# Kernel optimization log

Measured on AMD Instinct MI355X. Metric: run time of the kernel, lower is better.

## Reference

```python
import jax, jax.numpy as jnp
import numpy as np

BN_EPS = 1e-5


def setup_inputs() -> dict:
    key = jax.random.key(0)
    ks = jax.random.split(key, 9)
    B, C, H, W = 2, 64, 128, 128
    Ci = 32  # inter_channels
    sc = 0.05
    x = jax.random.normal(ks[0], (B, C, H, W), jnp.float32)
    g_w = jax.random.normal(ks[1], (Ci, C), jnp.float32) * sc
    g_b = jax.random.normal(ks[2], (Ci,), jnp.float32) * sc
    theta_w = jax.random.normal(ks[3], (Ci, C), jnp.float32) * sc
    theta_b = jax.random.normal(ks[4], (Ci,), jnp.float32) * sc
    phi_w = jax.random.normal(ks[5], (Ci, C), jnp.float32) * sc
    phi_b = jax.random.normal(ks[6], (Ci,), jnp.float32) * sc
    w_w = jax.random.normal(ks[7], (C, Ci), jnp.float32) * sc
    w_b = jnp.zeros((C,), jnp.float32)
    # BatchNorm affine params (random so the block is non-trivial; the torch
    # code zero-inits them, which would make the whole block an identity).
    bn_gamma = 1.0 + 0.1 * jax.random.normal(ks[8], (C,), jnp.float32)
    bn_beta = jnp.zeros((C,), jnp.float32)
    return dict(x=x, g_w=g_w, g_b=g_b, theta_w=theta_w, theta_b=theta_b,
                phi_w=phi_w, phi_b=phi_b, w_w=w_w, w_b=w_b,
                bn_gamma=bn_gamma, bn_beta=bn_beta)


def reference(x, g_w, g_b, theta_w, theta_b, phi_w, phi_b, w_w, w_b,
              bn_gamma, bn_beta):
    B, C, H, W = x.shape
    Ci = g_w.shape[0]
    H1, W1 = H // 2, W // 2

    def block(xq):  # embedded-gaussian non-local block on one quadrant group [B,C,h,w]
        b, c, h, w = xq.shape
        n = h * w
        xf = xq.reshape(b, c, n)                                  # [B,C,N]
        th = jnp.einsum('oc,bcn->bno', theta_w, xf) + theta_b     # [B,N,Ci]
        ph = jnp.einsum('oc,bcn->bon', phi_w, xf) + phi_b[:, None]  # [B,Ci,N]
        gx = jnp.einsum('oc,bcn->bno', g_w, xf) + g_b             # [B,N,Ci]
        f = jnp.einsum('bno,bom->bnm', th, ph)                    # [B,N,N] affinity
        a = jax.nn.softmax(f, axis=-1)
        y = jnp.einsum('bnm,bmo->bno', a, gx)                     # [B,N,Ci]
        wy = jnp.einsum('co,bno->bcn', w_w, y) + w_b[:, None]     # [B,C,N]
        wy = wy.reshape(b, c, h, w)
        # BatchNorm2d, training-mode batch stats (per quadrant call in torch)
        mu = wy.mean(axis=(0, 2, 3), keepdims=True)
        var = wy.var(axis=(0, 2, 3), keepdims=True)
        bn = (wy - mu) * jax.lax.rsqrt(var + BN_EPS)
        bn = bn * bn_gamma[None, :, None, None] + bn_beta[None, :, None, None]
        return bn + xq                                            # residual

    # split into 4 quadrants: [B,C,H,W] -> [4,B,C,H1,W1] (quadrant-major)
    xq = x.reshape(B, C, 2, H1, 2, W1).transpose(2, 4, 0, 1, 3, 5)
    xq = xq.reshape(4, B, C, H1, W1)
    zq = jax.vmap(block)(xq)                                      # [4,B,C,H1,W1]
    # reassemble
    z = zq.reshape(2, 2, B, C, H1, W1).transpose(2, 3, 0, 4, 1, 5)
    return z.reshape(B, C, H, W)
```

## Files before the change

### kernel.cpp

```cpp
#include <hip/hip_runtime.h>
#include <stdint.h>

typedef __bf16 bf16x8 __attribute__((ext_vector_type(8)));
typedef short  short4v __attribute__((ext_vector_type(4)));
typedef float  floatx4 __attribute__((ext_vector_type(4)));
typedef uint32_t u32x4 __attribute__((ext_vector_type(4)));

#define DI __device__ __forceinline__

DI uint16_t bf1(float a) {
    union { __bf16 h; uint16_t u; } r; r.h = (__bf16)a; return r.u;
}

__global__ __launch_bounds__(256) void proj_kernel(
    const float* __restrict__ x,
    const float* __restrict__ tw, const float* __restrict__ tb,
    const float* __restrict__ pw, const float* __restrict__ pb,
    const float* __restrict__ gw, const float* __restrict__ gb,
    uint16_t* __restrict__ th, uint16_t* __restrict__ phT,
    uint16_t* __restrict__ vP)
{
    __shared__ uint16_t ldsg[32 * 68];
    int nt = blockIdx.x & 63, blk = blockIdx.x >> 6;
    int tid = threadIdx.x, wid = tid >> 6, lane = tid & 63;
    int quad = lane >> 4, low = lane & 15;

    int b = blk & 1, q = blk >> 1, qh = q >> 1, qw = q & 1;
    int pixA = wid * 16 + low;
    const float* xg = x + (size_t)b * 1048576 +
                      (size_t)(qh * 64 + nt) * 128 + qw * 64 + pixA;

    float a0[8], a1[8];
#pragma unroll
    for (int j = 0; j < 8; ++j) {
        a0[j] = xg[(size_t)(quad * 8 + j) * 16384];
        a1[j] = xg[(size_t)(32 + quad * 8 + j) * 16384];
    }
    bf16x8 A0, A1;
#pragma unroll
    for (int j = 0; j < 8; ++j) {
        A0[j] = (__bf16)a0[j];
        A1[j] = (__bf16)a1[j];
    }

    auto dotile = [&](const float* W, const float* Bv, int o0) -> floatx4 {
        floatx4 acc;
        float bias = Bv[o0 + low];
#pragma unroll
        for (int r = 0; r < 4; ++r) acc[r] = bias;
        const float* wr = W + (o0 + low) * 64 + quad * 8;
        floatx4 w0a = *(const floatx4*)(wr);
        floatx4 w0b = *(const floatx4*)(wr + 4);
        floatx4 w1a = *(const floatx4*)(wr + 32);
        floatx4 w1b = *(const floatx4*)(wr + 36);
        bf16x8 B0, B1;
#pragma unroll
        for (int j = 0; j < 4; ++j) {
            B0[j]     = (__bf16)w0a[j];
            B0[j + 4] = (__bf16)w0b[j];
            B1[j]     = (__bf16)w1a[j];
            B1[j + 4] = (__bf16)w1b[j];
        }
        acc = __builtin_amdgcn_mfma_f32_16x16x32_bf16(A0, B0, acc, 0, 0, 0);
        acc = __builtin_amdgcn_mfma_f32_16x16x32_bf16(A1, B1, acc, 0, 0, 0);
        return acc;
    };

    size_t thbase = ((size_t)blk * 4096 + nt * 64 + wid * 16 + quad * 4) * 32;

    floatx4 t0 = dotile(tw, tb, 0), t1 = dotile(tw, tb, 16);
#pragma unroll
    for (int r = 0; r < 4; ++r) {
        th[thbase + r * 32 + low]      = bf1(t0[r] * 1.44269504088896f);
        th[thbase + r * 32 + 16 + low] = bf1(t1[r] * 1.44269504088896f);
    }
    floatx4 p0 = dotile(pw, pb, 0), p1 = dotile(pw, pb, 16);
#pragma unroll
    for (int r = 0; r < 4; ++r) {
        phT[thbase + r * 32 + low]      = bf1(p0[r]);
        phT[thbase + r * 32 + 16 + low] = bf1(p1[r]);
    }
    floatx4 g0 = dotile(gw, gb, 0), g1 = dotile(gw, gb, 16);
#pragma unroll
    for (int r = 0; r < 4; ++r) {
        ldsg[(low)      * 68 + wid * 16 + quad * 4 + r] = bf1(g0[r]);
        ldsg[(16 + low) * 68 + wid * 16 + quad * 4 + r] = bf1(g1[r]);
    }
    __syncthreads();
    {
        int o = tid >> 3, k = (tid & 7) * 8;
        const uint16_t* src = &ldsg[o * 68 + k];
        uint64_t lo = *(const uint64_t*)(src);
        uint64_t hi = *(const uint64_t*)(src + 4);
        union { uint64_t q[2]; u32x4 v; } out;
        out.q[0] = lo; out.q[1] = hi;
        *(u32x4*)(vP + (size_t)blk * 131072 + nt * 2048 + tid * 8) = out.v;
    }
}

__global__ __launch_bounds__(512, 4) void flash_kernel(
    const uint16_t* __restrict__ th, const uint16_t* __restrict__ phT,
    const uint16_t* __restrict__ vP, const float* __restrict__ w_w,
    const float* __restrict__ w_b, float* __restrict__ wy,
    float2* __restrict__ partials)
{
    __shared__ uint16_t ldsK[2][2][2][64 * 40];
    __shared__ uint16_t ldsV[2][2][2][32 * 72];
    __shared__ float sred[4][64][2];
    int blk = blockIdx.x & 7;
    int rg  = blockIdx.x >> 3;
    int tid = threadIdx.x, wid = tid >> 6, lane = tid & 63;
    int half = wid >> 2, w4 = wid & 3;
    int ltid = tid & 255;
    int quad = lane >> 4, low = lane & 15;
    int n0 = rg * 64 + w4 * 16;
    int sstag = wid & 1;

    const uint16_t* thB = th  + (size_t)blk * 131072;
    const uint16_t* kG  = phT + (size_t)blk * 131072;
    const uint16_t* vG  = vP  + (size_t)blk * 131072;

    bf16x8 qf = *(const bf16x8*)(thB + (n0 + low) * 32 + quad * 8);

    const int kWr = (ltid >> 2) * 40 + (ltid & 3) * 8;
    const int vWr = (ltid >> 3) * 72 + (ltid & 7) * 8;
    const u32x4* kSrc = (const u32x4*)kG + half * 8192 + ltid;
    const u32x4* vSrc = (const u32x4*)vG + half * 8192 + ltid;

    u32x4 kr0 = kSrc[0],  kr1 = kSrc[256];
    u32x4 vr0 = vSrc[0],  vr1 = vSrc[256];
    *(u32x4*)(&ldsK[half][0][0][kWr]) = kr0;  *(u32x4*)(&ldsK[half][0][1][kWr]) = kr1;
    *(u32x4*)(&ldsV[half][0][0][vWr]) = vr0;  *(u32x4*)(&ldsV[half][0][1][vWr]) = vr1;
    __syncthreads();

    floatx4 zero = {0.f, 0.f, 0.f, 0.f};
    floatx4 oa0 = zero, oa1 = zero, os = zero;
    union { uint32_t u[2]; short4v v; } ones;
    ones.u[0] = 0x3F803F80u; ones.u[1] = 0x3F803F80u;

    for (int t = 0; t < 16; ++t) {
        int buf = t & 1;
        if (t < 15) {
            kr0 = kSrc[(2*t + 2) * 256]; kr1 = kSrc[(2*t + 3) * 256];
            vr0 = vSrc[(2*t + 2) * 256]; vr1 = vSrc[(2*t + 3) * 256];
        }
#pragma unroll
        for (int si = 0; si < 2; ++si) {
            int s = si ^ sstag;
            const uint16_t* Kb = ldsK[half][buf][s];
            const uint16_t* Vb = ldsV[half][buf][s];
            bf16x8  kf[4]; short4v va[4], vb[4];
#pragma unroll
            for (int c = 0; c < 4; ++c) {
                kf[c] = *(const bf16x8*)(Kb + (c * 16 + low) * 40 + quad * 8);
                va[c] = *(const short4v*)(Vb + low * 72 + c * 16 + quad * 4);
                vb[c] = *(const short4v*)(Vb + (16 + low) * 72 + c * 16 + quad * 4);
            }
            floatx4 sa[4];
#pragma unroll
            for (int c = 0; c < 4; ++c)
                sa[c] = __builtin_amdgcn_mfma_f32_16x16x32_bf16(kf[c], qf, zero, 0, 0, 0);
            union { __bf16 h[4]; short4v v; } P[4];
#pragma unroll
            for (int c = 0; c < 4; ++c) {
                float p0 = __builtin_amdgcn_exp2f(sa[c][0]);
                float p1 = __builtin_amdgcn_exp2f(sa[c][1]);
                float p2 = __builtin_amdgcn_exp2f(sa[c][2]);
                float p3 = __builtin_amdgcn_exp2f(sa[c][3]);
                P[c].h[0] = (__bf16)p0; P[c].h[1] = (__bf16)p1;
                P[c].h[2] = (__bf16)p2; P[c].h[3] = (__bf16)p3;
            }
#pragma unroll
            for (int c = 0; c < 4; ++c) {
                oa0 = __builtin_amdgcn_mfma_f32_16x16x16bf16_1k(va[c], P[c].v, oa0, 0, 0, 0);
                oa1 = __builtin_amdgcn_mfma_f32_16x16x16bf16_1k(vb[c], P[c].v, oa1, 0, 0, 0);
                os  = __builtin_amdgcn_mfma_f32_16x16x16bf16_1k(ones.v, P[c].v, os, 0, 0, 0);
            }
        }
        if (t < 15) {
            *(u32x4*)(&ldsK[half][buf ^ 1][0][kWr]) = kr0;
            *(u32x4*)(&ldsK[half][buf ^ 1][1][kWr]) = kr1;
            *(u32x4*)(&ldsV[half][buf ^ 1][0][vWr]) = vr0;
            *(u32x4*)(&ldsV[half][buf ^ 1][1][vWr]) = vr1;
        }
        __syncthreads();
    }

    {
        float* exM = (float*)(&ldsK[half][0][0][0]);
        int li9 = ltid * 9;
#pragma unroll
        for (int r = 0; r < 4; ++r) {
            exM[li9 + r]     = oa0[r];
            exM[li9 + 4 + r] = oa1[r];
        }
        exM[li9 + 8] = os[0];
    }
    __syncthreads();
    const float* exO = (const float*)(&ldsK[half ^ 1][0][0][0]);
    float os0 = os[0] + exO[ltid * 9 + 8];
#pragma unroll
    for (int r = 0; r < 4; ++r) {
        oa0[r] += exO[ltid * 9 + r];
        oa1[r] += exO[ltid * 9 + 4 + r];
    }

    float rinv = 1.0f / os0;
    union { __bf16 h[4]; short4v v; } Y0, Y1;
#pragma unroll
    for (int r = 0; r < 4; ++r) {
        Y0.h[r] = (__bf16)(oa0[r] * rinv);
        Y1.h[r] = (__bf16)(oa1[r] * rinv);
    }

    float* wyB = wy + (size_t)blk * 262144;
    int n = n0 + low;
#pragma unroll
    for (int cc = 0; cc < 2; ++cc) {
        int ct = half * 2 + cc;
        floatx4 acc;
#pragma unroll
        for (int r = 0; r < 4; ++r) acc[r] = w_b[ct * 16 + quad * 4 + r];
        floatx4 w0 = *(const floatx4*)(w_w + (ct * 16 + low) * 32 + quad * 4);
        floatx4 w1 = *(const floatx4*)(w_w + (ct * 16 + low) * 32 + 16 + quad * 4);
        union { __bf16 h[4]; short4v v; } W0, W1;
#pragma unroll
        for (int r = 0; r < 4; ++r) {
            W0.h[r] = (__bf16)w0[r];
            W1.h[r] = (__bf16)w1[r];
        }
        acc = __builtin_amdgcn_mfma_f32_16x16x16bf16_1k(W0.v, Y0.v, acc, 0, 0, 0);
        acc = __builtin_amdgcn_mfma_f32_16x16x16bf16_1k(W1.v, Y1.v, acc, 0, 0, 0);
#pragma unroll
        for (int r = 0; r < 4; ++r) {
            wyB[(size_t)(ct * 16 + quad * 4 + r) * 4096 + n] = acc[r];
            float s = acc[r], ss = acc[r] * acc[r];
            s += __shfl_xor(s, 1); ss += __shfl_xor(ss, 1);
            s += __shfl_xor(s, 2); ss += __shfl_xor(ss, 2);
            s += __shfl_xor(s, 4); ss += __shfl_xor(ss, 4);
            s += __shfl_xor(s, 8); ss += __shfl_xor(ss, 8);
            if (low == 0) {
                sred[w4][ct * 16 + quad * 4 + r][0] = s;
                sred[w4][ct * 16 + quad * 4 + r][1] = ss;
            }
        }
    }
    __syncthreads();
    if (tid < 64) {
        float s  = sred[0][tid][0] + sred[1][tid][0] + sred[2][tid][0] + sred[3][tid][0];
        float ss = sred[0][tid][1] + sred[1][tid][1] + sred[2][tid][1] + sred[3][tid][1];
        partials[((size_t)blk * 64 + rg) * 64 + tid] = make_float2(s, ss);
    }
}

__global__ __launch_bounds__(256) void stats_kernel(
    const float2* __restrict__ partials, const float* __restrict__ gamma,
    const float* __restrict__ beta, float2* __restrict__ stats)
{
    int q = blockIdx.x;
    int c = threadIdx.x & 63, g = threadIdx.x >> 6;
    float S = 0.f, SS = 0.f;
    for (int w = g; w < 128; w += 4) {
        int wg = (q * 2 + (w >> 6)) * 64 + (w & 63);
        float2 p = partials[(size_t)wg * 64 + c];
        S += p.x; SS += p.y;
    }
    __shared__ float sh[2][4][64];
    sh[0][g][c] = S; sh[1][g][c] = SS;
    __syncthreads();
    if (threadIdx.x < 64) {
        int cc = threadIdx.x;
        float St  = sh[0][0][cc] + sh[0][1][cc] + sh[0][2][cc] + sh[0][3][cc];
        float SSt = sh[1][0][cc] + sh[1][1][cc] + sh[1][2][cc] + sh[1][3][cc];
        float mu  = St * (1.0f / 8192.0f);
        float var = SSt * (1.0f / 8192.0f) - mu * mu;
        float scale = gamma[cc] * rsqrtf(var + 1e-5f);
        float shift = beta[cc] - mu * scale;
        stats[q * 64 + cc] = make_float2(scale, shift);
    }
}

__global__ __launch_bounds__(256) void final_kernel(
    const float* __restrict__ wy, const float2* __restrict__ stats,
    const float* __restrict__ x, float* __restrict__ out)
{
    size_t base = ((size_t)blockIdx.x * 256 + threadIdx.x) * 4;
    int n   = (int)(base & 4095);
    int c   = (int)((base >> 12) & 63);
    int blk = (int)(base >> 18);
    int b = blk & 1, q = blk >> 1, qh = q >> 1, qw = q & 1;
    int i = n >> 6, j = n & 63;
    float2 sc = stats[q * 64 + c];
    floatx4 wv = *(const floatx4*)(wy + base);
    size_t xa = ((size_t)(b * 64 + c) * 128 + (qh * 64 + i)) * 128 + qw * 64 + j;
    floatx4 xv = *(const floatx4*)(x + xa);
    floatx4 ov;
#pragma unroll
    for (int k = 0; k < 4; ++k) ov[k] = wv[k] * sc.x + sc.y + xv[k];
    *(floatx4*)(out + xa) = ov;
}

extern "C" void kernel_launch(void* const* d_in, const int* in_sizes, int n_in,
                              void* d_out, int out_size, void* d_ws, size_t ws_size,
                              hipStream_t stream)
{
    const float* x       = (const float*)d_in[0];
    const float* g_w     = (const float*)d_in[1];
    const float* g_b     = (const float*)d_in[2];
    const float* theta_w = (const float*)d_in[3];
    const float* theta_b = (const float*)d_in[4];
    const float* phi_w   = (const float*)d_in[5];
    const float* phi_b   = (const float*)d_in[6];
    const float* w_w     = (const float*)d_in[7];
    const float* w_b     = (const float*)d_in[8];
    const float* gamma   = (const float*)d_in[9];
    const float* beta    = (const float*)d_in[10];

    char* ws = (char*)d_ws;
    uint16_t* th       = (uint16_t*)(ws);
    uint16_t* phT      = (uint16_t*)(ws + (2u << 20));
    uint16_t* vP       = (uint16_t*)(ws + (4u << 20));
    float*    wy       = (float*)(ws + (6u << 20));
    float2*   partials = (float2*)(ws + (14u << 20));
    float2*   stats    = (float2*)(ws + (14u << 20) + (1u << 18));

    proj_kernel  <<<512,  256, 0, stream>>>(x, theta_w, theta_b, phi_w, phi_b,
                                            g_w, g_b, th, phT, vP);
    flash_kernel <<<512,  512, 0, stream>>>(th, phT, vP, w_w, w_b, wy, partials);
    stats_kernel <<<4,    256, 0, stream>>>(partials, gamma, beta, stats);
    final_kernel <<<2048, 256, 0, stream>>>(wy, stats, x, (float*)d_out);
}
```

Measured before the change: 139.5 us.

## Process two query tiles per wave in flash kernel to reuse K/V fragments

Each wave now handles 32 query rows (two 16-row tiles) instead of 16, so every K and V fragment loaded from LDS feeds twice as many MFMAs. The grid is halved to 256 blocks and launch bounds are relaxed to allow more registers. The stats kernel is rewritten as one 64-thread block per channel/quadrant doing a shuffle reduction over the smaller partials array. The trade is fewer blocks and higher register pressure, which lowers occupancy on a 256-CU device, and the per-wave staggering of the LDS sub-tile order is removed.

```diff
diff --git a/kernel.cpp b/kernel.cpp
--- a/kernel.cpp
+++ b/kernel.cpp
@@ -98,7 +98,7 @@
     }
 }
 
-__global__ __launch_bounds__(512, 4) void flash_kernel(
+__global__ __launch_bounds__(512, 2) void flash_kernel(
     const uint16_t* __restrict__ th, const uint16_t* __restrict__ phT,
     const uint16_t* __restrict__ vP, const float* __restrict__ w_w,
     const float* __restrict__ w_b, float* __restrict__ wy,
@@ -113,14 +113,14 @@
     int half = wid >> 2, w4 = wid & 3;
     int ltid = tid & 255;
     int quad = lane >> 4, low = lane & 15;
-    int n0 = rg * 64 + w4 * 16;
-    int sstag = wid & 1;
+    int n0 = rg * 128 + w4 * 32;
 
     const uint16_t* thB = th  + (size_t)blk * 131072;
     const uint16_t* kG  = phT + (size_t)blk * 131072;
     const uint16_t* vG  = vP  + (size_t)blk * 131072;
 
-    bf16x8 qf = *(const bf16x8*)(thB + (n0 + low) * 32 + quad * 8);
+    bf16x8 qfA = *(const bf16x8*)(thB + (n0 + low) * 32 + quad * 8);
+    bf16x8 qfB = *(const bf16x8*)(thB + (n0 + 16 + low) * 32 + quad * 8);
 
     const int kWr = (ltid >> 2) * 40 + (ltid & 3) * 8;
     const int vWr = (ltid >> 3) * 72 + (ltid & 7) * 8;
@@ -134,7 +134,8 @@
     __syncthreads();
 
     floatx4 zero = {0.f, 0.f, 0.f, 0.f};
-    floatx4 oa0 = zero, oa1 = zero, os = zero;
+    floatx4 oaA0 = zero, oaA1 = zero, osA = zero;
+    floatx4 oaB0 = zero, oaB1 = zero, osB = zero;
     union { uint32_t u[2]; short4v v; } ones;
     ones.u[0] = 0x3F803F80u; ones.u[1] = 0x3F803F80u;
 
@@ -145,8 +146,7 @@
             vr0 = vSrc[(2*t + 2) * 256]; vr1 = vSrc[(2*t + 3) * 256];
         }
 #pragma unroll
-        for (int si = 0; si < 2; ++si) {
-            int s = si ^ sstag;
+        for (int s = 0; s < 2; ++s) {
             const uint16_t* Kb = ldsK[half][buf][s];
             const uint16_t* Vb = ldsV[half][buf][s];
             bf16x8  kf[4]; short4v va[4], vb[4];
@@ -156,25 +156,32 @@
                 va[c] = *(const short4v*)(Vb + low * 72 + c * 16 + quad * 4);
                 vb[c] = *(const short4v*)(Vb + (16 + low) * 72 + c * 16 + quad * 4);
             }
-            floatx4 sa[4];
-#pragma unroll
-            for (int c = 0; c < 4; ++c)
-                sa[c] = __builtin_amdgcn_mfma_f32_16x16x32_bf16(kf[c], qf, zero, 0, 0, 0);
-            union { __bf16 h[4]; short4v v; } P[4];
+            floatx4 saA[4], saB[4];
 #pragma unroll
             for (int c = 0; c < 4; ++c) {
-                float p0 = __builtin_amdgcn_exp2f(sa[c][0]);
-                float p1 = __builtin_amdgcn_exp2f(sa[c][1]);
-                float p2 = __builtin_amdgcn_exp2f(sa[c][2]);
-                float p3 = __builtin_amdgcn_exp2f(sa[c][3]);
-                P[c].h[0] = (__bf16)p0; P[c].h[1] = (__bf16)p1;
-                P[c].h[2] = (__bf16)p2; P[c].h[3] = (__bf16)p3;
-            }
+                saA[c] = __builtin_amdgcn_mfma_f32_16x16x32_bf16(kf[c], qfA, zero, 0, 0, 0);
+                saB[c] = __builtin_amdgcn_mfma_f32_16x16x32_bf16(kf[c], qfB, zero, 0, 0, 0);
+            }
+            union { __bf16 h[4]; short4v v; } PA[4], PB[4];
 #pragma unroll
             for (int c = 0; c < 4; ++c) {
-                oa0 = __builtin_amdgcn_mfma_f32_16x16x16bf16_1k(va[c], P[c].v, oa0, 0, 0, 0);
-                oa1 = __builtin_amdgcn_mfma_f32_16x16x16bf16_1k(vb[c], P[c].v, oa1, 0, 0, 0);
-                os  = __builtin_amdgcn_mfma_f32_16x16x16bf16_1k(ones.v, P[c].v, os, 0, 0, 0);
+                PA[c].h[0] = (__bf16)__builtin_amdgcn_exp2f(saA[c][0]);
+                PA[c].h[1] = (__bf16)__builtin_amdgcn_exp2f(saA[c][1]);
+                PA[c].h[2] = (__bf16)__builtin_amdgcn_exp2f(saA[c][2]);
+                PA[c].h[3] = (__bf16)__builtin_amdgcn_exp2f(saA[c][3]);
+                PB[c].h[0] = (__bf16)__builtin_amdgcn_exp2f(saB[c][0]);
+                PB[c].h[1] = (__bf16)__builtin_amdgcn_exp2f(saB[c][1]);
+                PB[c].h[2] = (__bf16)__builtin_amdgcn_exp2f(saB[c][2]);
+                PB[c].h[3] = (__bf16)__builtin_amdgcn_exp2f(saB[c][3]);
+            }
+#pragma unroll
+            for (int c = 0; c < 4; ++c) {
+                oaA0 = __builtin_amdgcn_mfma_f32_16x16x16bf16_1k(va[c], PA[c].v, oaA0, 0, 0, 0);
+                oaB0 = __builtin_amdgcn_mfma_f32_16x16x16bf16_1k(va[c], PB[c].v, oaB0, 0, 0, 0);
+                oaA1 = __builtin_amdgcn_mfma_f32_16x16x16bf16_1k(vb[c], PA[c].v, oaA1, 0, 0, 0);
+                oaB1 = __builtin_amdgcn_mfma_f32_16x16x16bf16_1k(vb[c], PB[c].v, oaB1, 0, 0, 0);
+                osA  = __builtin_amdgcn_mfma_f32_16x16x16bf16_1k(ones.v, PA[c].v, osA, 0, 0, 0);
+                osB  = __builtin_amdgcn_mfma_f32_16x16x16bf16_1k(ones.v, PB[c].v, osB, 0, 0, 0);
             }
         }
         if (t < 15) {
@@ -188,39 +195,50 @@
 
     {
         float* exM = (float*)(&ldsK[half][0][0][0]);
-        int li9 = ltid * 9;
+        int li = ltid * 18;
 #pragma unroll
         for (int r = 0; r < 4; ++r) {
-            exM[li9 + r]     = oa0[r];
-            exM[li9 + 4 + r] = oa1[r];
-        }
-        exM[li9 + 8] = os[0];
+            exM[li + r]      = oaA0[r];
+            exM[li + 4 + r]  = oaA1[r];
+            exM[li + 9 + r]  = oaB0[r];
+            exM[li + 13 + r] = oaB1[r];
+        }
+        exM[li + 8]  = osA[0];
+        exM[li + 17] = osB[0];
     }
     __syncthreads();
     const float* exO = (const float*)(&ldsK[half ^ 1][0][0][0]);
-    float os0 = os[0] + exO[ltid * 9 + 8];
-#pragma unroll
-    for (int r = 0; r < 4; ++r) {
-        oa0[r] += exO[ltid * 9 + r];
-        oa1[r] += exO[ltid * 9 + 4 + r];
-    }
-
-    float rinv = 1.0f / os0;
-    union { __bf16 h[4]; short4v v; } Y0, Y1;
-#pragma unroll
-    for (int r = 0; r < 4; ++r) {
-        Y0.h[r] = (__bf16)(oa0[r] * rinv);
-        Y1.h[r] = (__bf16)(oa1[r] * rinv);
+    float osA0 = osA[0] + exO[ltid * 18 + 8];
+    float osB0 = osB[0] + exO[ltid * 18 + 17];
+#pragma unroll
+    for (int r = 0; r < 4; ++r) {
+        oaA0[r] += exO[ltid * 18 + r];
+        oaA1[r] += exO[ltid * 18 + 4 + r];
+        oaB0[r] += exO[ltid * 18 + 9 + r];
+        oaB1[r] += exO[ltid * 18 + 13 + r];
+    }
+
+    float rinvA = 1.0f / osA0, rinvB = 1.0f / osB0;
+    union { __bf16 h[4]; short4v v; } YA0, YA1, YB0, YB1;
+#pragma unroll
+    for (int r = 0; r < 4; ++r) {
+        YA0.h[r] = (__bf16)(oaA0[r] * rinvA);
+        YA1.h[r] = (__bf16)(oaA1[r] * rinvA);
+        YB0.h[r] = (__bf16)(oaB0[r] * rinvB);
+        YB1.h[r] = (__bf16)(oaB1[r] * rinvB);
     }
 
     float* wyB = wy + (size_t)blk * 262144;
-    int n = n0 + low;
+    int nA = n0 + low, nB = n0 + 16 + low;
 #pragma unroll
     for (int cc = 0; cc < 2; ++cc) {
         int ct = half * 2 + cc;
-        floatx4 acc;
-#pragma unroll
-        for (int r = 0; r < 4; ++r) acc[r] = w_b[ct * 16 + quad * 4 + r];
+        floatx4 accA, accB;
+#pragma unroll
+        for (int r = 0; r < 4; ++r) {
+            accA[r] = w_b[ct * 16 + quad * 4 + r];
+            accB[r] = accA[r];
+        }
         floatx4 w0 = *(const floatx4*)(w_w + (ct * 16 + low) * 32 + quad * 4);
         floatx4 w1 = *(const floatx4*)(w_w + (ct * 16 + low) * 32 + 16 + quad * 4);
         union { __bf16 h[4]; short4v v; } W0, W1;
@@ -229,19 +247,24 @@
             W0.h[r] = (__bf16)w0[r];
             W1.h[r] = (__bf16)w1[r];
         }
-        acc = __builtin_amdgcn_mfma_f32_16x16x16bf16_1k(W0.v, Y0.v, acc, 0, 0, 0);
-        acc = __builtin_amdgcn_mfma_f32_16x16x16bf16_1k(W1.v, Y1.v, acc, 0, 0, 0);
+        accA = __builtin_amdgcn_mfma_f32_16x16x16bf16_1k(W0.v, YA0.v, accA, 0, 0, 0);
+        accA = __builtin_amdgcn_mfma_f32_16x16x16bf16_1k(W1.v, YA1.v, accA, 0, 0, 0);
+        accB = __builtin_amdgcn_mfma_f32_16x16x16bf16_1k(W0.v, YB0.v, accB, 0, 0, 0);
+        accB = __builtin_amdgcn_mfma_f32_16x16x16bf16_1k(W1.v, YB1.v, accB, 0, 0, 0);
 #pragma unroll
         for (int r = 0; r < 4; ++r) {
-            wyB[(size_t)(ct * 16 + quad * 4 + r) * 4096 + n] = acc[r];
-            float s = acc[r], ss = acc[r] * acc[r];
+            int ch = ct * 16 + quad * 4 + r;
+            wyB[(size_t)ch * 4096 + nA] = accA[r];
+            wyB[(size_t)ch * 4096 + nB] = accB[r];
+            float s = accA[r] + accB[r];
+            float ss = accA[r] * accA[r] + accB[r] * accB[r];
             s += __shfl_xor(s, 1); ss += __shfl_xor(ss, 1);
             s += __shfl_xor(s, 2); ss += __shfl_xor(ss, 2);
             s += __shfl_xor(s, 4); ss += __shfl_xor(ss, 4);
             s += __shfl_xor(s, 8); ss += __shfl_xor(ss, 8);
             if (low == 0) {
-                sred[w4][ct * 16 + quad * 4 + r][0] = s;
-                sred[w4][ct * 16 + quad * 4 + r][1] = ss;
+                sred[w4][ch][0] = s;
+                sred[w4][ch][1] = ss;
             }
         }
     }
@@ -249,34 +272,32 @@
     if (tid < 64) {
         float s  = sred[0][tid][0] + sred[1][tid][0] + sred[2][tid][0] + sred[3][tid][0];
         float ss = sred[0][tid][1] + sred[1][tid][1] + sred[2][tid][1] + sred[3][tid][1];
-        partials[((size_t)blk * 64 + rg) * 64 + tid] = make_float2(s, ss);
-    }
-}
-
-__global__ __launch_bounds__(256) void stats_kernel(
+        partials[((size_t)blk * 32 + rg) * 64 + tid] = make_float2(s, ss);
+    }
+}
+
+__global__ __launch_bounds__(64) void stats_kernel(
     const float2* __restrict__ partials, const float* __restrict__ gamma,
     const float* __restrict__ beta, float2* __restrict__ stats)
 {
-    int q = blockIdx.x;
-    int c = threadIdx.x & 63, g = threadIdx.x >> 6;
-    float S = 0.f, SS = 0.f;
-    for (int w = g; w < 128; w += 4) {
-        int wg = (q * 2 + (w >> 6)) * 64 + (w & 63);
-        float2 p = partials[(size_t)wg * 64 + c];
-        S += p.x; SS += p.y;
-    }
-    __shared__ float sh[2][4][64];
-    sh[0][g][c] = S; sh[1][g][c] = SS;
-    __syncthreads();
-    if (threadIdx.x < 64) {
-        int cc = threadIdx.x;
-        float St  = sh[0][0][cc] + sh[0][1][cc] + sh[0][2][cc] + sh[0][3][cc];
-        float SSt = sh[1][0][cc] + sh[1][1][cc] + sh[1][2][cc] + sh[1][3][cc];
-        float mu  = St * (1.0f / 8192.0f);
-        float var = SSt * (1.0f / 8192.0f) - mu * mu;
-        float scale = gamma[cc] * rsqrtf(var + 1e-5f);
-        float shift = beta[cc] - mu * scale;
-        stats[q * 64 + cc] = make_float2(scale, shift);
+    int q = blockIdx.x >> 6, c = blockIdx.x & 63;
+    int t = threadIdx.x;
+    int b = t >> 5, rg = t & 31;
+    int blk = q * 2 + b;
+    float2 p = partials[((size_t)blk * 32 + rg) * 64 + c];
+    float S = p.x, SS = p.y;
+    S += __shfl_xor(S, 1);  SS += __shfl_xor(SS, 1);
+    S += __shfl_xor(S, 2);  SS += __shfl_xor(SS, 2);
+    S += __shfl_xor(S, 4);  SS += __shfl_xor(SS, 4);
+    S += __shfl_xor(S, 8);  SS += __shfl_xor(SS, 8);
+    S += __shfl_xor(S, 16); SS += __shfl_xor(SS, 16);
+    S += __shfl_xor(S, 32); SS += __shfl_xor(SS, 32);
+    if (t == 0) {
+        float mu  = S * (1.0f / 8192.0f);
+        float var = SS * (1.0f / 8192.0f) - mu * mu;
+        float scale = gamma[c] * rsqrtf(var + 1e-5f);
+        float shift = beta[c] - mu * scale;
+        stats[q * 64 + c] = make_float2(scale, shift);
     }
 }
 
@@ -326,7 +347,7 @@
 
     proj_kernel  <<<512,  256, 0, stream>>>(x, theta_w, theta_b, phi_w, phi_b,
                                             g_w, g_b, th, phT, vP);
-    flash_kernel <<<512,  512, 0, stream>>>(th, phT, vP, w_w, w_b, wy, partials);
-    stats_kernel <<<4,    256, 0, stream>>>(partials, gamma, beta, stats);
+    flash_kernel <<<256,  512, 0, stream>>>(th, phT, vP, w_w, w_b, wy, partials);
+    stats_kernel <<<256,  64,  0, stream>>>(partials, gamma, beta, stats);
     final_kernel <<<2048, 256, 0, stream>>>(wy, stats, x, (float*)d_out);
 }
```

After: 128.1 us. 1.09x faster.
